# Optimization experiments

Hardware: AMD Instinct MI355X
Metric: run time of the kernel (lower is better)

## Reference

```python
import jax, jax.numpy as jnp
import numpy as np

N_NODES = 10000
N_EDGES = 320000
K = 5
C_IN = 128
C_OUT = 128


def setup_inputs() -> dict:
    key = jax.random.key(0)
    k_h, k_x, k_w, k_b = jax.random.split(key, 4)
    h = jax.random.normal(k_h, (N_NODES, C_IN), dtype=jnp.float32)
    X = jax.random.normal(k_x, (N_EDGES, K), dtype=jnp.float32)
    weight = jax.random.normal(k_w, (K, C_IN, C_OUT), dtype=jnp.float32) * 0.05
    bias = jax.random.normal(k_b, (C_OUT,), dtype=jnp.float32)
    # Unique (src, dst) pairs so scatter-set == segment-sum (matches torch indexing assignment).
    rng = np.random.default_rng(0)
    lin = np.unique(rng.integers(0, N_NODES * N_NODES, size=int(N_EDGES * 1.3)))
    assert len(lin) >= N_EDGES
    lin = lin[:N_EDGES]
    edge_index = jnp.asarray(np.stack([lin // N_NODES, lin % N_NODES]), dtype=jnp.int64)
    batch_node = jnp.zeros((N_NODES,), dtype=jnp.float32)
    return {"h": h, "X": X, "edge_index": edge_index, "batch_node": batch_node,
            "weight": weight, "bias": bias}


def reference(h, X, edge_index, batch_node, weight, bias):
    # Original torch code scatters X.T into a dense (K, N, N) adjacency and does
    # res = A @ h; that equals, per order k:
    #   res[k, i, :] = sum_{e: src_e = i} X[e, k] * h[dst_e, :]
    # which we compute sparsely with segment_sum (edges are unique).
    N = h.shape[0]
    src = edge_index[0]
    dst = edge_index[1]
    h_dst = h[dst]  # [E, C_in] gathered destination features

    def per_k(xk):  # xk: [E] edge values for one order k
        return jax.ops.segment_sum(xk[:, None] * h_dst, src, num_segments=N)  # [N, C_in]

    res_k = jax.vmap(per_k, in_axes=1)(X)  # [K, N, C_in]
    out = jnp.einsum('kni,kio->no', res_k, weight) + bias  # [N, C_out]
    return out
```

## Files before the change

kernel.cpp:

```cpp
#include <hip/hip_runtime.h>

#define N_NODES 10000
#define N_EDGES 320000
#define KDIM 640
#define C_OUT 128

typedef __attribute__((ext_vector_type(8))) short short8;
typedef __attribute__((ext_vector_type(4))) float floatx4;
typedef __attribute__((ext_vector_type(2))) unsigned int uintx2;

__device__ __forceinline__ unsigned short f2bf(float f) {
    unsigned int b = __float_as_uint(f);
    b = (b + 0x7FFFu + ((b >> 16) & 1u)) >> 16;
    return (unsigned short)b;
}
__device__ __forceinline__ unsigned int pack2(float x, float y) {
    return (unsigned int)f2bf(x) | ((unsigned int)f2bf(y) << 16);
}
__device__ __forceinline__ float2 unpack2(unsigned int u) {
    float2 r;
    r.x = __uint_as_float(u << 16);
    r.y = __uint_as_float(u & 0xFFFF0000u);
    return r;
}

__global__ __launch_bounds__(256) void prep(
        const float* __restrict__ h, uintx2* __restrict__ hb4,
        const float* __restrict__ W, unsigned short* __restrict__ Wt,
        const int* __restrict__ src, int* __restrict__ offsets) {
    const int bid = blockIdx.x;
    const int tid = threadIdx.x;

    if (bid < 1250) {
        const int t = bid * 256 + tid;
        floatx4 v = __builtin_nontemporal_load(&((const floatx4*)h)[t]);
        uintx2 o;
        o.x = pack2(v.x, v.y);
        o.y = pack2(v.z, v.w);
        hb4[t] = o;
    } else if (bid < 1330) {
        __shared__ float tile[32][33];
        const int b = bid - 1250;
        const int k0 = (b % 20) * 32, o0 = (b / 20) * 32;
        const int tx = tid & 31, ty = tid >> 5;
#pragma unroll
        for (int i = 0; i < 4; ++i)
            tile[ty + 8 * i][tx] =
                __builtin_nontemporal_load(&W[(size_t)(k0 + ty + 8 * i) * C_OUT + o0 + tx]);
        __syncthreads();
#pragma unroll
        for (int i = 0; i < 4; ++i)
            Wt[(size_t)(o0 + ty + 8 * i) * KDIM + k0 + tx] = f2bf(tile[tx][ty + 8 * i]);
    } else {
        const int n = (bid - 1330) * 256 + tid;
        if (n > N_NODES) return;
        int lo = 0, hi = N_EDGES;
        while (lo < hi) {
            int mid = (lo + hi) >> 1;
            if (src[mid] < n) lo = mid + 1; else hi = mid;
        }
        offsets[n] = lo;
    }
}

__global__ __launch_bounds__(512, 4) void fused_spectconv(
        const unsigned int* __restrict__ h2,
        const float* __restrict__ X,
        const int* __restrict__ dst,
        const int* __restrict__ offsets,
        const unsigned short* __restrict__ Wt,
        const float* __restrict__ bias,
        float* __restrict__ out) {
    __shared__ unsigned short Rs[16][648];
    __shared__ unsigned short Bs[128][68];

    const int tid  = threadIdx.x;
    const int wv   = __builtin_amdgcn_readfirstlane(tid >> 6);
    const int lane = tid & 63;
    const int m0   = blockIdx.x * 16;

    for (int nn = 0; nn < 2; ++nn) {
        const int node = m0 + wv * 2 + nn;
        const int e0 = offsets[node];
        const int e1 = offsets[node + 1];

        float a0x=0,a0y=0, a1x=0,a1y=0, a2x=0,a2y=0, a3x=0,a3y=0, a4x=0,a4y=0;

        int e = e0;
        for (; e + 7 < e1; e += 8) {
            int d[8];
            unsigned int u[8];
#pragma unroll
            for (int q = 0; q < 8; ++q) d[q] = dst[e + q];
#pragma unroll
            for (int q = 0; q < 8; ++q)
                u[q] = h2[(size_t)d[q] * 64 + lane];
#pragma unroll
            for (int q = 0; q < 8; ++q) {
                const float* Xp = X + (size_t)(e + q) * 5;
                const float x0 = Xp[0], x1 = Xp[1], x2 = Xp[2], x3 = Xp[3], x4 = Xp[4];
                const float2 hv = unpack2(u[q]);
                a0x = fmaf(x0, hv.x, a0x); a0y = fmaf(x0, hv.y, a0y);
                a1x = fmaf(x1, hv.x, a1x); a1y = fmaf(x1, hv.y, a1y);
                a2x = fmaf(x2, hv.x, a2x); a2y = fmaf(x2, hv.y, a2y);
                a3x = fmaf(x3, hv.x, a3x); a3y = fmaf(x3, hv.y, a3y);
                a4x = fmaf(x4, hv.x, a4x); a4y = fmaf(x4, hv.y, a4y);
            }
        }
        for (; e < e1; ++e) {
            const int d = dst[e];
            const unsigned int u = h2[(size_t)d * 64 + lane];
            const float* Xp = X + (size_t)e * 5;
            const float x0 = Xp[0], x1 = Xp[1], x2 = Xp[2], x3 = Xp[3], x4 = Xp[4];
            const float2 hv = unpack2(u);
            a0x = fmaf(x0, hv.x, a0x); a0y = fmaf(x0, hv.y, a0y);
            a1x = fmaf(x1, hv.x, a1x); a1y = fmaf(x1, hv.y, a1y);
            a2x = fmaf(x2, hv.x, a2x); a2y = fmaf(x2, hv.y, a2y);
            a3x = fmaf(x3, hv.x, a3x); a3y = fmaf(x3, hv.y, a3y);
            a4x = fmaf(x4, hv.x, a4x); a4y = fmaf(x4, hv.y, a4y);
        }

        const int nrel = wv * 2 + nn;
        *(unsigned int*)&Rs[nrel][0 * 128 + 2 * lane] = pack2(a0x, a0y);
        *(unsigned int*)&Rs[nrel][1 * 128 + 2 * lane] = pack2(a1x, a1y);
        *(unsigned int*)&Rs[nrel][2 * 128 + 2 * lane] = pack2(a2x, a2y);
        *(unsigned int*)&Rs[nrel][3 * 128 + 2 * lane] = pack2(a3x, a3y);
        *(unsigned int*)&Rs[nrel][4 * 128 + 2 * lane] = pack2(a4x, a4y);
    }

    __syncthreads();

    const int col  = lane & 15;
    const int quad = lane >> 4;
    const int c0   = wv * 16;

    floatx4 acc = {0.f, 0.f, 0.f, 0.f};

#pragma unroll
    for (int chunk = 0; chunk < 10; ++chunk) {
        if (chunk) __syncthreads();
#pragma unroll
        for (int r = 0; r < 2; ++r) {
            const int c = r * 512 + tid;
            const int row = c >> 3, c8 = c & 7;
            *(short8*)&Bs[row][c8 * 8] =
                *(const short8*)(Wt + (size_t)row * KDIM + chunk * 64 + c8 * 8);
        }
        __syncthreads();

#pragma unroll
        for (int hh = 0; hh < 2; ++hh) {
            const short8 af = *(const short8*)&Rs[col][chunk * 64 + hh * 32 + quad * 8];
            const short8 bf = *(const short8*)&Bs[c0 + col][hh * 32 + quad * 8];
            acc = __builtin_amdgcn_mfma_f32_16x16x32_bf16(af, bf, acc, 0, 0, 0);
        }
    }

    const float bv = bias[c0 + col];
#pragma unroll
    for (int r = 0; r < 4; ++r) {
        const int m = m0 + quad * 4 + r;
        __builtin_nontemporal_store(acc[r] + bv, &out[(size_t)m * C_OUT + c0 + col]);
    }
}

extern "C" void kernel_launch(void* const* d_in, const int* in_sizes, int n_in,
                              void* d_out, int out_size, void* d_ws, size_t ws_size,
                              hipStream_t stream) {
    const float* h      = (const float*)d_in[0];
    const float* X      = (const float*)d_in[1];
    const int*   ei     = (const int*)d_in[2];
    const float* weight = (const float*)d_in[4];
    const float* bias   = (const float*)d_in[5];
    float* out = (float*)d_out;

    const int* src = ei;
    const int* dst = ei + N_EDGES;

    char* wsb = (char*)d_ws;
    int*            offsets = (int*)wsb;
    uintx2*         hb4     = (uintx2*)(wsb + (64 << 10));
    unsigned short* Wtb     = (unsigned short*)(wsb + (64 << 10) + (4 << 20));

    prep<<<1370, 256, 0, stream>>>(h, hb4, weight, Wtb, src, offsets);
    fused_spectconv<<<625, 512, 0, stream>>>((const unsigned int*)hb4, X, dst,
                                             offsets, Wtb, bias, out);
}
```

Baseline: 100.9 us.

## Software-pipeline edge gathers and register-prefetch weight chunks in fused kernel

The edge aggregation loop now issues the dst index and h gather loads for the next group of 8 edges before doing the FMAs on the current group, so memory latency overlaps with arithmetic. In the GEMM phase, each weight chunk is prefetched into registers while MFMAs run on the chunk already in shared memory, then written to shared memory between barriers. The first weight chunk is staged before the existing sync, which also covers the Rs writes. This costs more live registers under the 512-thread, 4-block launch bound and could cause spilling.

Result: no change. 99.86 us (-1.0%).

```diff
diff --git a/kernel.cpp b/kernel.cpp
--- a/kernel.cpp
+++ b/kernel.cpp
@@ -63,6 +63,21 @@
     }
 }
 
+__device__ __forceinline__ void edge_fma8(const float* __restrict__ X, int e,
+                                          const unsigned int* u, float2* a) {
+#pragma unroll
+    for (int q = 0; q < 8; ++q) {
+        const float* Xp = X + (size_t)(e + q) * 5;
+        const float x0 = Xp[0], x1 = Xp[1], x2 = Xp[2], x3 = Xp[3], x4 = Xp[4];
+        const float2 hv = unpack2(u[q]);
+        a[0].x = fmaf(x0, hv.x, a[0].x); a[0].y = fmaf(x0, hv.y, a[0].y);
+        a[1].x = fmaf(x1, hv.x, a[1].x); a[1].y = fmaf(x1, hv.y, a[1].y);
+        a[2].x = fmaf(x2, hv.x, a[2].x); a[2].y = fmaf(x2, hv.y, a[2].y);
+        a[3].x = fmaf(x3, hv.x, a[3].x); a[3].y = fmaf(x3, hv.y, a[3].y);
+        a[4].x = fmaf(x4, hv.x, a[4].x); a[4].y = fmaf(x4, hv.y, a[4].y);
+    }
+}
+
 __global__ __launch_bounds__(512, 4) void fused_spectconv(
         const unsigned int* __restrict__ h2,
         const float* __restrict__ X,
@@ -84,75 +99,91 @@
         const int e0 = offsets[node];
         const int e1 = offsets[node + 1];
 
-        float a0x=0,a0y=0, a1x=0,a1y=0, a2x=0,a2y=0, a3x=0,a3y=0, a4x=0,a4y=0;
+        float2 a[5] = {{0.f,0.f},{0.f,0.f},{0.f,0.f},{0.f,0.f},{0.f,0.f}};
 
         int e = e0;
-        for (; e + 7 < e1; e += 8) {
-            int d[8];
-            unsigned int u[8];
+        int d[8]; unsigned int u[8];
+        const bool have = (e + 7 < e1);
+        if (have) {
 #pragma unroll
             for (int q = 0; q < 8; ++q) d[q] = dst[e + q];
 #pragma unroll
             for (int q = 0; q < 8; ++q)
                 u[q] = h2[(size_t)d[q] * 64 + lane];
-#pragma unroll
-            for (int q = 0; q < 8; ++q) {
-                const float* Xp = X + (size_t)(e + q) * 5;
-                const float x0 = Xp[0], x1 = Xp[1], x2 = Xp[2], x3 = Xp[3], x4 = Xp[4];
-                const float2 hv = unpack2(u[q]);
-                a0x = fmaf(x0, hv.x, a0x); a0y = fmaf(x0, hv.y, a0y);
-                a1x = fmaf(x1, hv.x, a1x); a1y = fmaf(x1, hv.y, a1y);
-                a2x = fmaf(x2, hv.x, a2x); a2y = fmaf(x2, hv.y, a2y);
-                a3x = fmaf(x3, hv.x, a3x); a3y = fmaf(x3, hv.y, a3y);
-                a4x = fmaf(x4, hv.x, a4x); a4y = fmaf(x4, hv.y, a4y);
-            }
+        }
+        for (; e + 15 < e1; e += 8) {
+            int dn[8]; unsigned int un[8];
+#pragma unroll
+            for (int q = 0; q < 8; ++q) dn[q] = dst[e + 8 + q];
+#pragma unroll
+            for (int q = 0; q < 8; ++q)
+                un[q] = h2[(size_t)dn[q] * 64 + lane];
+            edge_fma8(X, e, u, a);
+#pragma unroll
+            for (int q = 0; q < 8; ++q) u[q] = un[q];
+        }
+        if (have) {
+            edge_fma8(X, e, u, a);
+            e += 8;
         }
         for (; e < e1; ++e) {
-            const int d = dst[e];
-            const unsigned int u = h2[(size_t)d * 64 + lane];
+            const int dd = dst[e];
+            const unsigned int uu = h2[(size_t)dd * 64 + lane];
             const float* Xp = X + (size_t)e * 5;
             const float x0 = Xp[0], x1 = Xp[1], x2 = Xp[2], x3 = Xp[3], x4 = Xp[4];
-            const float2 hv = unpack2(u);
-            a0x = fmaf(x0, hv.x, a0x); a0y = fmaf(x0, hv.y, a0y);
-            a1x = fmaf(x1, hv.x, a1x); a1y = fmaf(x1, hv.y, a1y);
-            a2x = fmaf(x2, hv.x, a2x); a2y = fmaf(x2, hv.y, a2y);
-            a3x = fmaf(x3, hv.x, a3x); a3y = fmaf(x3, hv.y, a3y);
-            a4x = fmaf(x4, hv.x, a4x); a4y = fmaf(x4, hv.y, a4y);
+            const float2 hv = unpack2(uu);
+            a[0].x = fmaf(x0, hv.x, a[0].x); a[0].y = fmaf(x0, hv.y, a[0].y);
+            a[1].x = fmaf(x1, hv.x, a[1].x); a[1].y = fmaf(x1, hv.y, a[1].y);
+            a[2].x = fmaf(x2, hv.x, a[2].x); a[2].y = fmaf(x2, hv.y, a[2].y);
+            a[3].x = fmaf(x3, hv.x, a[3].x); a[3].y = fmaf(x3, hv.y, a[3].y);
+            a[4].x = fmaf(x4, hv.x, a[4].x); a[4].y = fmaf(x4, hv.y, a[4].y);
         }
 
         const int nrel = wv * 2 + nn;
-        *(unsigned int*)&Rs[nrel][0 * 128 + 2 * lane] = pack2(a0x, a0y);
-        *(unsigned int*)&Rs[nrel][1 * 128 + 2 * lane] = pack2(a1x, a1y);
-        *(unsigned int*)&Rs[nrel][2 * 128 + 2 * lane] = pack2(a2x, a2y);
-        *(unsigned int*)&Rs[nrel][3 * 128 + 2 * lane] = pack2(a3x, a3y);
-        *(unsigned int*)&Rs[nrel][4 * 128 + 2 * lane] = pack2(a4x, a4y);
-    }
-
-    __syncthreads();
+        *(unsigned int*)&Rs[nrel][0 * 128 + 2 * lane] = pack2(a[0].x, a[0].y);
+        *(unsigned int*)&Rs[nrel][1 * 128 + 2 * lane] = pack2(a[1].x, a[1].y);
+        *(unsigned int*)&Rs[nrel][2 * 128 + 2 * lane] = pack2(a[2].x, a[2].y);
+        *(unsigned int*)&Rs[nrel][3 * 128 + 2 * lane] = pack2(a[3].x, a[3].y);
+        *(unsigned int*)&Rs[nrel][4 * 128 + 2 * lane] = pack2(a[4].x, a[4].y);
+    }
 
     const int col  = lane & 15;
     const int quad = lane >> 4;
     const int c0   = wv * 16;
 
+    const int srow = tid >> 3;
+    const int sseg = (tid & 7) * 8;
+    const unsigned short* wp0 = Wt + (size_t)srow * KDIM + sseg;
+    const unsigned short* wp1 = wp0 + (size_t)64 * KDIM;
+
+    {
+        const short8 g0 = *(const short8*)wp0;
+        const short8 g1 = *(const short8*)wp1;
+        *(short8*)&Bs[srow][sseg]      = g0;
+        *(short8*)&Bs[64 + srow][sseg] = g1;
+    }
+    __syncthreads();
+
     floatx4 acc = {0.f, 0.f, 0.f, 0.f};
 
 #pragma unroll
     for (int chunk = 0; chunk < 10; ++chunk) {
-        if (chunk) __syncthreads();
-#pragma unroll
-        for (int r = 0; r < 2; ++r) {
-            const int c = r * 512 + tid;
-            const int row = c >> 3, c8 = c & 7;
-            *(short8*)&Bs[row][c8 * 8] =
-                *(const short8*)(Wt + (size_t)row * KDIM + chunk * 64 + c8 * 8);
-        }
-        __syncthreads();
-
+        short8 n0, n1;
+        if (chunk < 9) {
+            n0 = *(const short8*)(wp0 + (chunk + 1) * 64);
+            n1 = *(const short8*)(wp1 + (chunk + 1) * 64);
+        }
 #pragma unroll
         for (int hh = 0; hh < 2; ++hh) {
             const short8 af = *(const short8*)&Rs[col][chunk * 64 + hh * 32 + quad * 8];
             const short8 bf = *(const short8*)&Bs[c0 + col][hh * 32 + quad * 8];
             acc = __builtin_amdgcn_mfma_f32_16x16x32_bf16(af, bf, acc, 0, 0, 0);
+        }
+        if (chunk < 9) {
+            __syncthreads();
+            *(short8*)&Bs[srow][sseg]      = n0;
+            *(short8*)&Bs[64 + srow][sseg] = n1;
+            __syncthreads();
         }
     }
 
```
